# Kernel optimization log

Measured on AMD Instinct MI355X. Metric: run time of the kernel, lower is better.

## Reference

```python
import jax, jax.numpy as jnp
import numpy as np

NEG_BIG = -9e15
ALPHA = 0.1  # leaky relu slope


def setup_inputs() -> dict:
    key = jax.random.key(0)
    k1, k2, k3, k4 = jax.random.split(key, 4)
    B, C, N, F = 4, 4, 2048, 64
    x = jax.random.normal(k1, (B, C, N, F), dtype=jnp.float32)
    adj = jax.random.randint(k2, (N, N), 0, 2, dtype=jnp.int32)
    # xavier_uniform on shape (1,1,F,1): fan_in=1, fan_out=F -> bound = 1.414*sqrt(6/(1+F))
    bound = 1.414 * np.sqrt(6.0 / (1.0 + F))
    a1 = jax.random.uniform(k3, (F, 1), jnp.float32, -bound, bound)
    a2 = jax.random.uniform(k4, (F, 1), jnp.float32, -bound, bound)
    return {"x": x, "adj": adj, "a1": a1, "a2": a2}


def reference(x, adj, a1, a2):
    # x: [B, C, N, F]; adj: [N, N]; a1, a2: [F, 1]
    h = x
    f1 = jnp.einsum("bcnf,fo->bcn", h, a1)  # [B, C, N]
    f2 = jnp.einsum("bcnf,fo->bcn", h, a2)  # [B, C, N]
    e = f1[..., :, None] + f2[..., None, :]  # [B, C, N, N] additive scores
    e = jnp.where(e > 0, e, ALPHA * e)       # leaky relu
    e = jnp.where(adj[None, None] > 0, e, jnp.float32(NEG_BIG))
    attention = jax.nn.softmax(e, axis=-1)
    # dropout is identity in eval mode (training=False)
    return jnp.matmul(attention, h)          # [B, C, N, F]
```

## Files before the change

kernel.cpp:

```cpp
#include <hip/hip_runtime.h>
#include <hip/hip_bf16.h>
#include <cstdint>

#define NN 2048
#define FF 64
#define BCC 16

typedef float f32x4 __attribute__((ext_vector_type(4)));
typedef int   i32x4 __attribute__((ext_vector_type(4)));
typedef _Float16 half8 __attribute__((ext_vector_type(8)));
typedef uint32_t u32x4 __attribute__((ext_vector_type(4)));


__global__ __launch_bounds__(256) void k_prep(const float* __restrict__ x,
        const int* __restrict__ adj,
        const float* __restrict__ a1, const float* __restrict__ a2,
        _Float16* __restrict__ xP, _Float16* __restrict__ Uh,
        _Float16* __restrict__ Vh, _Float16* __restrict__ CIh,
        unsigned char* __restrict__ ADJP) {
    __shared__ float tile[32][65];
    __shared__ float red[2][32][8];
    int tid = threadIdx.x;

    #pragma unroll
    for (int tt = 0; tt < 2; tt++) {
        int t  = blockIdx.x * 2 + tt;
        int bc = t >> 6;
        int n0 = (t & 63) * 32;
        int row = tid >> 3;
        int fo  = (tid & 7) * 8;

        const float* xr = x + ((size_t)bc * NN + n0 + row) * FF + fo;
        f32x4 v0 = *(const f32x4*)xr;
        f32x4 v1 = *(const f32x4*)(xr + 4);
        *(f32x4*)&tile[row][fo]     = v0;
        *(f32x4*)&tile[row][fo + 4] = v1;

        f32x4 a1v0 = *(const f32x4*)(a1 + fo);
        f32x4 a1v1 = *(const f32x4*)(a1 + fo + 4);
        f32x4 a2v0 = *(const f32x4*)(a2 + fo);
        f32x4 a2v1 = *(const f32x4*)(a2 + fo + 4);
        float d1 = 0.f, d2 = 0.f;
        #pragma unroll
        for (int e = 0; e < 4; e++) {
            d1 += v0[e] * a1v0[e] + v1[e] * a1v1[e];
            d2 += v0[e] * a2v0[e] + v1[e] * a2v1[e];
        }
        red[0][row][tid & 7] = d1;
        red[1][row][tid & 7] = d2;
        __syncthreads();

        {
            int nb = tid >> 6, lane = tid & 63;
            int g = lane >> 4, l15 = lane & 15;
            half8 val;
            #pragma unroll
            for (int e = 0; e < 8; e++)
                val[e] = (_Float16)tile[8 * g + e][nb * 16 + l15];
            ((half8*)xP)[(((size_t)bc * 64 + (n0 >> 5)) * 4 + nb) * 64 + lane] = val;
        }
        if (tid < 32) {
            float f1 = 0.f, f2 = 0.f;
            #pragma unroll
            for (int s = 0; s < 8; s++) { f1 += red[0][tid][s]; f2 += red[1][tid][s]; }
            int idx = bc * NN + n0 + tid;
            Uh[idx]  = (_Float16)expf(f2);
            Vh[idx]  = (_Float16)expf(0.1f * f2);
            CIh[idx] = (_Float16)expf(-0.9f * f1);
        }
        __syncthreads();
    }

    {
        int wid  = tid >> 6, lane = tid & 63;
        int row  = blockIdx.x * 4 + wid;
        const int* ar = adj + (size_t)row * NN;
        unsigned char* ap = ADJP + (size_t)row * 256;
        #pragma unroll
        for (int m = 0; m < 4; m++) {
            int o = lane + 64 * m;
            const int* pj = ar + 8 * o;
            i32x4 w0 = *(const i32x4*)pj;
            i32x4 w1 = *(const i32x4*)(pj + 4);
            uint32_t b = 0;
            #pragma unroll
            for (int e = 0; e < 4; e++) {
                b |= (w0[e] > 0 ? 1u : 0u) << e;
                b |= (w1[e] > 0 ? 1u : 0u) << (e + 4);
            }
            ap[(o & 3) * 64 + (o >> 2)] = (unsigned char)b;
        }
    }
}

__global__ __launch_bounds__(256) void k_main(
        const _Float16* __restrict__ xP, const _Float16* __restrict__ Uh,
        const _Float16* __restrict__ Vh, const _Float16* __restrict__ CIh,
        const unsigned char* __restrict__ ADJP, float* __restrict__ out) {
    __shared__ _Float16 su[2048];
    __shared__ _Float16 sv[2048];
    __shared__ u32x4 lut[256];
    __shared__ float part[4][16][68];
    __shared__ float zp[4][16];

    int tid = threadIdx.x;
    int jq = tid >> 6, lane = tid & 63;
    int l15 = lane & 15, g = lane >> 4;

    int xcd = blockIdx.x & 7, kk = blockIdx.x >> 3;
    int bc   = (xcd << 1) | (kk >> 5);
    int iblk = kk & 31;
    int i0   = iblk * 64;

    ((u32x4*)su)[tid] = ((const u32x4*)(Uh + bc * NN))[tid];
    ((u32x4*)sv)[tid] = ((const u32x4*)(Vh + bc * NN))[tid];
    {
        uint32_t bb = tid;
        u32x4 lv;
        #pragma unroll
        for (int w = 0; w < 4; w++)
            lv[w] = (((bb >> (2 * w)) & 1u) ? 0xFFFFu : 0u)
                  | (((bb >> (2 * w + 1)) & 1u) ? 0xFFFF0000u : 0u);
        lut[bb] = lv;
    }
    const unsigned char* ab = ADJP + g * 64 + jq * 16;
    u32x4 adjw0 = *(const u32x4*)(ab + (size_t)(i0 + l15) * 256);
    u32x4 adjw1 = *(const u32x4*)(ab + (size_t)(i0 + 16 + l15) * 256);
    u32x4 adjw2 = *(const u32x4*)(ab + (size_t)(i0 + 32 + l15) * 256);
    u32x4 adjw3 = *(const u32x4*)(ab + (size_t)(i0 + 48 + l15) * 256);
    _Float16 Ci0 = CIh[bc * NN + i0 + l15];
    _Float16 Ci1 = CIh[bc * NN + i0 + 16 + l15];
    _Float16 Ci2 = CIh[bc * NN + i0 + 32 + l15];
    _Float16 Ci3 = CIh[bc * NN + i0 + 48 + l15];
    __syncthreads();

    f32x4 acc[4][4];
    #pragma unroll
    for (int a = 0; a < 4; a++)
        #pragma unroll
        for (int nb = 0; nb < 4; nb++)
            acc[a][nb] = (f32x4){0.f, 0.f, 0.f, 0.f};
    f32x4 accz[4];
    #pragma unroll
    for (int a = 0; a < 4; a++) accz[a] = (f32x4){0.f, 0.f, 0.f, 0.f};
    half8 onesh;
    #pragma unroll
    for (int e = 0; e < 8; e++) onesh[e] = (_Float16)1.0f;

    const u32x4* xPbc = (const u32x4*)xP + (size_t)bc * 16384;

    u32x4 A_x0, A_x1, A_x2, A_x3, B_x0, B_x1, B_x2, B_x3;

#define LOADX(P, J) do {                                                      \
        const u32x4* xw_ = xPbc + (((size_t)(jq * 16 + (J))) << 8) + lane;    \
        P##x0 = xw_[0]; P##x1 = xw_[64]; P##x2 = xw_[128]; P##x3 = xw_[192];  \
    } while (0)

#define GEN(AF, ADJW, CI) do {                                                \
        uint32_t b_ = (ADJW[(J_) >> 2] >> (((J_) & 3) * 8)) & 0xffu;          \
        u32x4 mm_ = lut[b_];                                                  \
        half8 mx_ = __builtin_elementwise_max(uu_, vv_ * (CI));               \
        AF = __builtin_bit_cast(half8, __builtin_bit_cast(u32x4, mx_) & mm_); \
    } while (0)

#define COMP(P, J) do {                                                       \
        const int J_ = (J);                                                   \
        const int jo_ = (jq * 16 + J_) * 32 + 8 * g;                          \
        half8 uu_ = *(const half8*)&su[jo_];                                  \
        half8 vv_ = *(const half8*)&sv[jo_];                                  \
        half8 af0_, af1_, af2_, af3_;                                         \
        GEN(af0_, adjw0, Ci0); GEN(af1_, adjw1, Ci1);                         \
        GEN(af2_, adjw2, Ci2); GEN(af3_, adjw3, Ci3);                         \
        half8 b0_ = __builtin_bit_cast(half8, P##x0);                         \
        half8 b1_ = __builtin_bit_cast(half8, P##x1);                         \
        half8 b2_ = __builtin_bit_cast(half8, P##x2);                         \
        half8 b3_ = __builtin_bit_cast(half8, P##x3);                         \
        __builtin_amdgcn_s_setprio(1);                                        \
        acc[0][0] = __builtin_amdgcn_mfma_f32_16x16x32_f16(af0_, b0_, acc[0][0], 0, 0, 0); \
        acc[0][1] = __builtin_amdgcn_mfma_f32_16x16x32_f16(af0_, b1_, acc[0][1], 0, 0, 0); \
        acc[0][2] = __builtin_amdgcn_mfma_f32_16x16x32_f16(af0_, b2_, acc[0][2], 0, 0, 0); \
        acc[0][3] = __builtin_amdgcn_mfma_f32_16x16x32_f16(af0_, b3_, acc[0][3], 0, 0, 0); \
        accz[0]   = __builtin_amdgcn_mfma_f32_16x16x32_f16(af0_, onesh, accz[0], 0, 0, 0); \
        acc[1][0] = __builtin_amdgcn_mfma_f32_16x16x32_f16(af1_, b0_, acc[1][0], 0, 0, 0); \
        acc[1][1] = __builtin_amdgcn_mfma_f32_16x16x32_f16(af1_, b1_, acc[1][1], 0, 0, 0); \
        acc[1][2] = __builtin_amdgcn_mfma_f32_16x16x32_f16(af1_, b2_, acc[1][2], 0, 0, 0); \
        acc[1][3] = __builtin_amdgcn_mfma_f32_16x16x32_f16(af1_, b3_, acc[1][3], 0, 0, 0); \
        accz[1]   = __builtin_amdgcn_mfma_f32_16x16x32_f16(af1_, onesh, accz[1], 0, 0, 0); \
        acc[2][0] = __builtin_amdgcn_mfma_f32_16x16x32_f16(af2_, b0_, acc[2][0], 0, 0, 0); \
        acc[2][1] = __builtin_amdgcn_mfma_f32_16x16x32_f16(af2_, b1_, acc[2][1], 0, 0, 0); \
        acc[2][2] = __builtin_amdgcn_mfma_f32_16x16x32_f16(af2_, b2_, acc[2][2], 0, 0, 0); \
        acc[2][3] = __builtin_amdgcn_mfma_f32_16x16x32_f16(af2_, b3_, acc[2][3], 0, 0, 0); \
        accz[2]   = __builtin_amdgcn_mfma_f32_16x16x32_f16(af2_, onesh, accz[2], 0, 0, 0); \
        acc[3][0] = __builtin_amdgcn_mfma_f32_16x16x32_f16(af3_, b0_, acc[3][0], 0, 0, 0); \
        acc[3][1] = __builtin_amdgcn_mfma_f32_16x16x32_f16(af3_, b1_, acc[3][1], 0, 0, 0); \
        acc[3][2] = __builtin_amdgcn_mfma_f32_16x16x32_f16(af3_, b2_, acc[3][2], 0, 0, 0); \
        acc[3][3] = __builtin_amdgcn_mfma_f32_16x16x32_f16(af3_, b3_, acc[3][3], 0, 0, 0); \
        accz[3]   = __builtin_amdgcn_mfma_f32_16x16x32_f16(af3_, onesh, accz[3], 0, 0, 0); \
        __builtin_amdgcn_s_setprio(0);                                        \
    } while (0)

    LOADX(A_, 0);
    LOADX(B_, 1);  COMP(A_, 0);
    LOADX(A_, 2);  COMP(B_, 1);
    LOADX(B_, 3);  COMP(A_, 2);
    LOADX(A_, 4);  COMP(B_, 3);
    LOADX(B_, 5);  COMP(A_, 4);
    LOADX(A_, 6);  COMP(B_, 5);
    LOADX(B_, 7);  COMP(A_, 6);
    LOADX(A_, 8);  COMP(B_, 7);
    LOADX(B_, 9);  COMP(A_, 8);
    LOADX(A_, 10); COMP(B_, 9);
    LOADX(B_, 11); COMP(A_, 10);
    LOADX(A_, 12); COMP(B_, 11);
    LOADX(B_, 13); COMP(A_, 12);
    LOADX(A_, 14); COMP(B_, 13);
    LOADX(B_, 15); COMP(A_, 14);
    COMP(B_, 15);
#undef LOADX
#undef GEN
#undef COMP

    float* outp = out + ((size_t)bc * NN + i0) * FF;
    #pragma unroll
    for (int a = 0; a < 4; a++) {
        #pragma unroll
        for (int nb = 0; nb < 4; nb++)
            #pragma unroll
            for (int r = 0; r < 4; r++)
                part[jq][4 * g + r][nb * 16 + l15] = acc[a][nb][r];
        if (l15 == 0) {
            #pragma unroll
            for (int r = 0; r < 4; r++)
                zp[jq][4 * g + r] = accz[a][r];
        }
        __syncthreads();
        #pragma unroll
        for (int rr = 0; rr < 4; rr++) {
            int row = jq * 4 + rr;
            float s = part[0][row][lane] + part[1][row][lane]
                    + part[2][row][lane] + part[3][row][lane];
            float z = zp[0][row] + zp[1][row] + zp[2][row] + zp[3][row];
            outp[(size_t)(16 * a + row) * FF + lane] = s / z;
        }
        __syncthreads();
    }
}

extern "C" void kernel_launch(void* const* d_in, const int* in_sizes, int n_in,
                              void* d_out, int out_size, void* d_ws, size_t ws_size,
                              hipStream_t stream) {
    const float* x  = (const float*)d_in[0];
    const int* adj  = (const int*)d_in[1];
    const float* a1 = (const float*)d_in[2];
    const float* a2 = (const float*)d_in[3];
    float* out = (float*)d_out;

    char* ws = (char*)d_ws;
    _Float16* xP  = (_Float16*)ws;
    _Float16* Uh  = (_Float16*)(ws + 4194304);
    _Float16* Vh  = (_Float16*)(ws + 4259840);
    _Float16* CIh = (_Float16*)(ws + 4325376);
    unsigned char* ADJP = (unsigned char*)(ws + 4390912);

    k_prep<<<512, 256, 0, stream>>>(x, adj, a1, a2, xP, Uh, Vh, CIh, ADJP);
    k_main<<<512, 256, 0, stream>>>(xP, Uh, Vh, CIh, ADJP, out);
}
```

Measured before the change: 25.98 us.

## Fuse prep and main kernels with atomic-counter grid dependencies

Merges the preprocessing and attention kernels into one persistent-style kernel. Each block preprocesses the x tile and adjacency rows that other blocks need, then spins on per-bc and per-row-block atomic counters until its dependencies are ready. This removes a kernel launch boundary and the full grid barrier between the two stages, and shares shared memory through a union. The cost is a memset launch for the counters and a deadlock risk if all 512 blocks cannot be co-resident, which launch_bounds(256,2) is meant to help ensure.

```diff
diff --git a/kernel.cpp b/kernel.cpp
--- a/kernel.cpp
+++ b/kernel.cpp
@@ -11,30 +11,41 @@
 typedef _Float16 half8 __attribute__((ext_vector_type(8)));
 typedef uint32_t u32x4 __attribute__((ext_vector_type(4)));
 
-
-__global__ __launch_bounds__(256) void k_prep(const float* __restrict__ x,
-        const int* __restrict__ adj,
+#define CNT_OFF 4915200
+
+union SmemU {
+    struct { float tile[32][65]; float red[2][32][8]; } p;
+    struct { _Float16 su[2048]; _Float16 sv[2048]; u32x4 lut[256];
+             float part[4][16][68]; float zp[4][16]; } m;
+};
+
+__global__ __launch_bounds__(256, 2) void k_fused(
+        const float* __restrict__ x, const int* __restrict__ adj,
         const float* __restrict__ a1, const float* __restrict__ a2,
         _Float16* __restrict__ xP, _Float16* __restrict__ Uh,
         _Float16* __restrict__ Vh, _Float16* __restrict__ CIh,
-        unsigned char* __restrict__ ADJP) {
-    __shared__ float tile[32][65];
-    __shared__ float red[2][32][8];
+        unsigned char* __restrict__ ADJP, unsigned* __restrict__ cnt,
+        float* __restrict__ out) {
+    __shared__ SmemU sm;
     int tid = threadIdx.x;
 
+    int xcd = blockIdx.x & 7, kk = blockIdx.x >> 3;
+    int bc   = (xcd << 1) | (kk >> 5);
+    int iblk = kk & 31;
+    int i0   = iblk * 64;
+
     #pragma unroll
     for (int tt = 0; tt < 2; tt++) {
-        int t  = blockIdx.x * 2 + tt;
-        int bc = t >> 6;
-        int n0 = (t & 63) * 32;
+        int jt = iblk * 2 + tt;
+        int n0 = jt * 32;
         int row = tid >> 3;
         int fo  = (tid & 7) * 8;
 
         const float* xr = x + ((size_t)bc * NN + n0 + row) * FF + fo;
         f32x4 v0 = *(const f32x4*)xr;
         f32x4 v1 = *(const f32x4*)(xr + 4);
-        *(f32x4*)&tile[row][fo]     = v0;
-        *(f32x4*)&tile[row][fo + 4] = v1;
+        *(f32x4*)&sm.p.tile[row][fo]     = v0;
+        *(f32x4*)&sm.p.tile[row][fo + 4] = v1;
 
         f32x4 a1v0 = *(const f32x4*)(a1 + fo);
         f32x4 a1v1 = *(const f32x4*)(a1 + fo + 4);
@@ -46,8 +57,8 @@
             d1 += v0[e] * a1v0[e] + v1[e] * a1v1[e];
             d2 += v0[e] * a2v0[e] + v1[e] * a2v1[e];
         }
-        red[0][row][tid & 7] = d1;
-        red[1][row][tid & 7] = d2;
+        sm.p.red[0][row][tid & 7] = d1;
+        sm.p.red[1][row][tid & 7] = d2;
         __syncthreads();
 
         {
@@ -56,13 +67,13 @@
             half8 val;
             #pragma unroll
             for (int e = 0; e < 8; e++)
-                val[e] = (_Float16)tile[8 * g + e][nb * 16 + l15];
-            ((half8*)xP)[(((size_t)bc * 64 + (n0 >> 5)) * 4 + nb) * 64 + lane] = val;
+                val[e] = (_Float16)sm.p.tile[8 * g + e][nb * 16 + l15];
+            ((half8*)xP)[(((size_t)bc * 64 + jt) * 4 + nb) * 64 + lane] = val;
         }
         if (tid < 32) {
             float f1 = 0.f, f2 = 0.f;
             #pragma unroll
-            for (int s = 0; s < 8; s++) { f1 += red[0][tid][s]; f2 += red[1][tid][s]; }
+            for (int s = 0; s < 8; s++) { f1 += sm.p.red[0][tid][s]; f2 += sm.p.red[1][tid][s]; }
             int idx = bc * NN + n0 + tid;
             Uh[idx]  = (_Float16)expf(f2);
             Vh[idx]  = (_Float16)expf(0.1f * f2);
@@ -73,7 +84,7 @@
 
     {
         int wid  = tid >> 6, lane = tid & 63;
-        int row  = blockIdx.x * 4 + wid;
+        int row  = iblk * 64 + bc * 4 + wid;
         const int* ar = adj + (size_t)row * NN;
         unsigned char* ap = ADJP + (size_t)row * 256;
         #pragma unroll
@@ -91,29 +102,23 @@
             ap[(o & 3) * 64 + (o >> 2)] = (unsigned char)b;
         }
     }
-}
-
-__global__ __launch_bounds__(256) void k_main(
-        const _Float16* __restrict__ xP, const _Float16* __restrict__ Uh,
-        const _Float16* __restrict__ Vh, const _Float16* __restrict__ CIh,
-        const unsigned char* __restrict__ ADJP, float* __restrict__ out) {
-    __shared__ _Float16 su[2048];
-    __shared__ _Float16 sv[2048];
-    __shared__ u32x4 lut[256];
-    __shared__ float part[4][16][68];
-    __shared__ float zp[4][16];
-
-    int tid = threadIdx.x;
+
+    __syncthreads();
+    if (tid == 0) {
+        __threadfence();
+        atomicAdd(&cnt[bc], 1u);
+        atomicAdd(&cnt[16 + iblk], 1u);
+        while (atomicAdd(&cnt[bc], 0u) < 32u)        __builtin_amdgcn_s_sleep(2);
+        while (atomicAdd(&cnt[16 + iblk], 0u) < 16u) __builtin_amdgcn_s_sleep(2);
+        __threadfence();
+    }
+    __syncthreads();
+
     int jq = tid >> 6, lane = tid & 63;
     int l15 = lane & 15, g = lane >> 4;
 
-    int xcd = blockIdx.x & 7, kk = blockIdx.x >> 3;
-    int bc   = (xcd << 1) | (kk >> 5);
-    int iblk = kk & 31;
-    int i0   = iblk * 64;
-
-    ((u32x4*)su)[tid] = ((const u32x4*)(Uh + bc * NN))[tid];
-    ((u32x4*)sv)[tid] = ((const u32x4*)(Vh + bc * NN))[tid];
+    ((u32x4*)sm.m.su)[tid] = ((const u32x4*)(Uh + bc * NN))[tid];
+    ((u32x4*)sm.m.sv)[tid] = ((const u32x4*)(Vh + bc * NN))[tid];
     {
         uint32_t bb = tid;
         u32x4 lv;
@@ -121,7 +126,7 @@
         for (int w = 0; w < 4; w++)
             lv[w] = (((bb >> (2 * w)) & 1u) ? 0xFFFFu : 0u)
                   | (((bb >> (2 * w + 1)) & 1u) ? 0xFFFF0000u : 0u);
-        lut[bb] = lv;
+        sm.m.lut[bb] = lv;
     }
     const unsigned char* ab = ADJP + g * 64 + jq * 16;
     u32x4 adjw0 = *(const u32x4*)(ab + (size_t)(i0 + l15) * 256);
@@ -158,7 +163,7 @@
 
 #define GEN(AF, ADJW, CI) do {                                                \
         uint32_t b_ = (ADJW[(J_) >> 2] >> (((J_) & 3) * 8)) & 0xffu;          \
-        u32x4 mm_ = lut[b_];                                                  \
+        u32x4 mm_ = sm.m.lut[b_];                                             \
         half8 mx_ = __builtin_elementwise_max(uu_, vv_ * (CI));               \
         AF = __builtin_bit_cast(half8, __builtin_bit_cast(u32x4, mx_) & mm_); \
     } while (0)
@@ -166,8 +171,8 @@
 #define COMP(P, J) do {                                                       \
         const int J_ = (J);                                                   \
         const int jo_ = (jq * 16 + J_) * 32 + 8 * g;                          \
-        half8 uu_ = *(const half8*)&su[jo_];                                  \
-        half8 vv_ = *(const half8*)&sv[jo_];                                  \
+        half8 uu_ = *(const half8*)&sm.m.su[jo_];                             \
+        half8 vv_ = *(const half8*)&sm.m.sv[jo_];                             \
         half8 af0_, af1_, af2_, af3_;                                         \
         GEN(af0_, adjw0, Ci0); GEN(af1_, adjw1, Ci1);                         \
         GEN(af2_, adjw2, Ci2); GEN(af3_, adjw3, Ci3);                         \
@@ -227,19 +232,20 @@
         for (int nb = 0; nb < 4; nb++)
             #pragma unroll
             for (int r = 0; r < 4; r++)
-                part[jq][4 * g + r][nb * 16 + l15] = acc[a][nb][r];
+                sm.m.part[jq][4 * g + r][nb * 16 + l15] = acc[a][nb][r];
         if (l15 == 0) {
             #pragma unroll
             for (int r = 0; r < 4; r++)
-                zp[jq][4 * g + r] = accz[a][r];
+                sm.m.zp[jq][4 * g + r] = accz[a][r];
         }
         __syncthreads();
         #pragma unroll
         for (int rr = 0; rr < 4; rr++) {
             int row = jq * 4 + rr;
-            float s = part[0][row][lane] + part[1][row][lane]
-                    + part[2][row][lane] + part[3][row][lane];
-            float z = zp[0][row] + zp[1][row] + zp[2][row] + zp[3][row];
+            float s = sm.m.part[0][row][lane] + sm.m.part[1][row][lane]
+                    + sm.m.part[2][row][lane] + sm.m.part[3][row][lane];
+            float z = sm.m.zp[0][row] + sm.m.zp[1][row]
+                    + sm.m.zp[2][row] + sm.m.zp[3][row];
             outp[(size_t)(16 * a + row) * FF + lane] = s / z;
         }
         __syncthreads();
@@ -261,7 +267,9 @@
     _Float16* Vh  = (_Float16*)(ws + 4259840);
     _Float16* CIh = (_Float16*)(ws + 4325376);
     unsigned char* ADJP = (unsigned char*)(ws + 4390912);
-
-    k_prep<<<512, 256, 0, stream>>>(x, adj, a1, a2, xP, Uh, Vh, CIh, ADJP);
-    k_main<<<512, 256, 0, stream>>>(xP, Uh, Vh, CIh, ADJP, out);
+    unsigned* cnt = (unsigned*)(ws + CNT_OFF);
+
+    hipMemsetAsync(cnt, 0, 48 * sizeof(unsigned), stream);
+    k_fused<<<512, 256, 0, stream>>>(x, adj, a1, a2, xP, Uh, Vh, CIh, ADJP,
+                                     cnt, out);
 }
```

Result: slower. 82.07 us (+215.9%).
